# Optimization experiments

Hardware: AMD Instinct MI355X
Metric: run time of the kernel (lower is better)

The kernel has to match this reference:

```python
import jax, jax.numpy as jnp
import numpy as np

H = 16
D_MODEL = 1024
D_K = D_MODEL // H
NEG = -1e9


def setup_inputs() -> dict:
    key = jax.random.key(0)
    ks = jax.random.split(key, 12)
    B, S, D = 2, 2048, D_MODEL
    scale = 1.0 / np.sqrt(D)
    inp = {
        "query": jax.random.normal(ks[0], (B, S, D), jnp.float32),
        "key": jax.random.normal(ks[1], (B, S, D), jnp.float32),
        "value": jax.random.normal(ks[2], (B, S, D), jnp.float32),
        "mask": jax.random.randint(ks[3], (B, S, S), 0, 2, jnp.int32),
        # four Linear(d_model, d_model) layers: q, k, v, out projections
        "Wq": jax.random.normal(ks[4], (D, D), jnp.float32) * scale,
        "bq": jnp.zeros((D,), jnp.float32),
        "Wk": jax.random.normal(ks[5], (D, D), jnp.float32) * scale,
        "bk": jnp.zeros((D,), jnp.float32),
        "Wv": jax.random.normal(ks[6], (D, D), jnp.float32) * scale,
        "bv": jnp.zeros((D,), jnp.float32),
        "Wo": jax.random.normal(ks[7], (D, D), jnp.float32) * scale,
        "bo": jnp.zeros((D,), jnp.float32),
    }
    return inp


def reference(query, key, value, mask, Wq, bq, Wk, bk, Wv, bv, Wo, bo):
    B, S, D = query.shape
    # QKV projections, then split into heads: [B, H, S, D_K]
    def proj(x, W, b):
        return (x @ W + b).reshape(B, S, H, D_K).transpose(0, 2, 1, 3)

    q = proj(query, Wq, bq)
    k = proj(key, Wk, bk)
    v = proj(value, Wv, bv)

    # scaled dot-product attention; scale by sqrt(d_k) (query.size(-1) after split)
    scores = jnp.einsum("bhqd,bhkd->bhqk", q, k) / np.sqrt(D_K)
    scores = jnp.where(mask[:, None, :, :] == 0, NEG, scores)
    p = jax.nn.softmax(scores, axis=-1)  # dropout is identity in eval mode
    x = jnp.einsum("bhqk,bhkd->bhqd", p, v)

    # merge heads and apply output projection
    x = x.transpose(0, 2, 1, 3).reshape(B, S, H * D_K)
    return x @ Wo + bo
```

## Files before the change

### kernel.cpp

```cpp
#include <hip/hip_runtime.h>

typedef _Float16 f16;
typedef __attribute__((ext_vector_type(2))) _Float16 f16x2;
typedef __attribute__((ext_vector_type(4))) _Float16 f16x4;
typedef __attribute__((ext_vector_type(8))) _Float16 f16x8;
typedef __attribute__((ext_vector_type(4))) float f32x4;

#define MFMA16(A_, B_, C_) __builtin_amdgcn_mfma_f32_16x16x32_f16(A_, B_, C_, 0, 0, 0)
#define EXP2(x) __builtin_amdgcn_exp2f(x)

#define NHEAD 16
#define SEQ 2048
#define DM 1024
#define DK 64
#define NBATCH 2
#define M_TOT (NBATCH * SEQ)
#define CSC 0.18033688011112042f

#define GLDS(gp, lp)                                                                     \
    __builtin_amdgcn_global_load_lds((const __attribute__((address_space(1))) void*)(gp), \
                                     (__attribute__((address_space(3))) void*)(lp), 16, 0, 0)

__global__ __launch_bounds__(256) void prep_k(
    const int* __restrict__ mask, unsigned long long* __restrict__ mp,
    const float* __restrict__ xq, const float* __restrict__ xk, const float* __restrict__ xv,
    f16* __restrict__ oq, f16* __restrict__ ok, f16* __restrict__ ov,
    const float* __restrict__ Wq, const float* __restrict__ Wk,
    const float* __restrict__ Wv, const float* __restrict__ Wo, f16* __restrict__ Wt) {
    __shared__ float T[64][65];
    const int z = blockIdx.z, bx = blockIdx.x, tid = threadIdx.x;
    if (z < 3) {
        const float* src = z == 0 ? xq : (z == 1 ? xk : xv);
        f16* dst = z == 0 ? oq : (z == 1 ? ok : ov);
        size_t i = ((size_t)bx * 256 + tid) * 8;
        float4 a = *(const float4*)&src[i];
        float4 b = *(const float4*)&src[i + 4];
        f16x8 h;
        h[0] = (f16)a.x; h[1] = (f16)a.y; h[2] = (f16)a.z; h[3] = (f16)a.w;
        h[4] = (f16)b.x; h[5] = (f16)b.y; h[6] = (f16)b.z; h[7] = (f16)b.w;
        *(f16x8*)&dst[i] = h;
    } else if (z == 3) {
        if (bx >= 1024) return;
        const int zz = bx >> 8, t = bx & 255;
        const float* W = zz == 0 ? Wq : (zz == 1 ? Wk : (zz == 2 ? Wv : Wo));
        const float wsc = zz == 0 ? CSC : 1.0f;
        f16* out = Wt + (size_t)zz * DM * DM;
        const int k0 = (t >> 4) * 64, n0 = (t & 15) * 64;
        const int r = tid >> 2, q = tid & 3;
        const float4* s = (const float4*)&W[(size_t)(k0 + r) * DM + n0 + q * 16];
        float4 v0 = s[0], v1 = s[1], v2 = s[2], v3 = s[3];
        T[r][q * 16 + 0] = v0.x; T[r][q * 16 + 1] = v0.y; T[r][q * 16 + 2] = v0.z; T[r][q * 16 + 3] = v0.w;
        T[r][q * 16 + 4] = v1.x; T[r][q * 16 + 5] = v1.y; T[r][q * 16 + 6] = v1.z; T[r][q * 16 + 7] = v1.w;
        T[r][q * 16 + 8] = v2.x; T[r][q * 16 + 9] = v2.y; T[r][q * 16 + 10] = v2.z; T[r][q * 16 + 11] = v2.w;
        T[r][q * 16 + 12] = v3.x; T[r][q * 16 + 13] = v3.y; T[r][q * 16 + 14] = v3.z; T[r][q * 16 + 15] = v3.w;
        __syncthreads();
        f16x8 h0, h1;
#pragma unroll
        for (int j = 0; j < 8; ++j) {
            h0[j] = (f16)(T[q * 16 + j][r] * wsc);
            h1[j] = (f16)(T[q * 16 + 8 + j][r] * wsc);
        }
        *(f16x8*)&out[(size_t)(n0 + r) * DM + k0 + q * 16] = h0;
        *(f16x8*)&out[(size_t)(n0 + r) * DM + k0 + q * 16 + 8] = h1;
    } else {
        if (bx >= 512) return;
        int lane = tid & 63;
        int gw = (bx * 256 + tid) >> 6;
        const int nw = (512 * 256) >> 6;
        const int nwords = NBATCH * SEQ * (SEQ / 64);
        for (int w = gw; w < nwords; w += nw) {
            int v = mask[(size_t)w * 64 + lane];
            unsigned long long bits = __ballot(v != 0);
            if (lane == 0) mp[w] = bits;
        }
    }
}

__device__ __forceinline__ void gemm_core(const f16* __restrict__ A, const f16* __restrict__ Bt,
                                          int m0, int n0, f16* Al, f16* Bl, f32x4 acc[4][4], int tid) {
    const int lane = tid & 63;
    const int wv = tid >> 6;
    const int wr = wv >> 1, wc = wv & 1;
    const int g = lane >> 4, c = lane & 15;

    for (int k0 = 0; k0 < DM; k0 += 64) {
#pragma unroll
        for (int j = 0; j < 4; ++j) {
            int chunk = j * 256 + tid;
            int row = chunk >> 3, cc = chunk & 7;
            int ccs = cc ^ (row & 7);
            GLDS(&A[(size_t)(m0 + row) * DM + k0 + ccs * 8], &Al[chunk * 8]);
        }
#pragma unroll
        for (int j = 0; j < 4; ++j) {
            int chunk = j * 256 + tid;
            int row = chunk >> 3, cc = chunk & 7;
            int ccs = cc ^ (row & 7);
            GLDS(&Bt[(size_t)(n0 + row) * DM + k0 + ccs * 8], &Bl[chunk * 8]);
        }
        __syncthreads();
#pragma unroll
        for (int ks = 0; ks < 2; ++ks) {
            f16x8 af[4], bf[4];
#pragma unroll
            for (int mi = 0; mi < 4; ++mi) {
                int row = wr * 64 + mi * 16 + c;
                af[mi] = *(const f16x8*)&Al[row * 64 + ((ks * 4 + g) ^ (row & 7)) * 8];
            }
#pragma unroll
            for (int ni = 0; ni < 4; ++ni) {
                int row = wc * 64 + ni * 16 + c;
                bf[ni] = *(const f16x8*)&Bl[row * 64 + ((ks * 4 + g) ^ (row & 7)) * 8];
            }
#pragma unroll
            for (int mi = 0; mi < 4; ++mi)
#pragma unroll
                for (int ni = 0; ni < 4; ++ni)
                    acc[mi][ni] = MFMA16(af[mi], bf[ni], acc[mi][ni]);
        }
        __syncthreads();
    }
}

__device__ __forceinline__ void xcd_swizzle(int& bx, int& by, int gdx) {
    int lin = by * gdx + bx;
    int nl = (lin & 7) * 32 + (lin >> 3);
    bx = nl % gdx;
    by = nl / gdx;
}

__global__ __launch_bounds__(256) void gemm_qkv2_k(
    const f16* __restrict__ Xq, const f16* __restrict__ Xk, const f16* __restrict__ Xv,
    const f16* __restrict__ Wt, const float* __restrict__ bq, const float* __restrict__ bk,
    const float* __restrict__ bv, f16* __restrict__ Qh, f16* __restrict__ Kh, f16* __restrict__ VhT) {
    __shared__ f16 Al[128 * 64];
    __shared__ f16 Bl[128 * 64];
    const int which = blockIdx.z;
    const f16* A = which == 0 ? Xq : (which == 1 ? Xk : Xv);
    const f16* Bt = Wt + (size_t)which * DM * DM;
    const float* bias = which == 0 ? bq : (which == 1 ? bk : bv);

    const int tid = threadIdx.x, lane = tid & 63, wv = tid >> 6;
    const int wr = wv >> 1, wc = wv & 1, g = lane >> 4, c = lane & 15;
    int bx = blockIdx.x, by = blockIdx.y;
    xcd_swizzle(bx, by, gridDim.x);
    const int m0 = by * 128, n0 = bx * 128;

    f32x4 acc[4][4] = {};
    gemm_core(A, Bt, m0, n0, Al, Bl, acc, tid);

    const float bsc = which == 0 ? CSC : 1.0f;
    if (which == 2) {
#pragma unroll
        for (int ni = 0; ni < 4; ++ni) {
            int n = n0 + wc * 64 + ni * 16 + c;
            float bias_n = bias[n];
            int hh = n >> 6, d = n & 63;
#pragma unroll
            for (int mi = 0; mi < 4; ++mi) {
                int mbase = m0 + wr * 64 + mi * 16 + g * 4;
                int bb = mbase >> 11, s = mbase & (SEQ - 1);
                f16x4 o;
#pragma unroll
                for (int r = 0; r < 4; ++r) o[r] = (f16)(acc[mi][ni][r] + bias_n);
                *(f16x4*)&VhT[(((size_t)(bb * NHEAD + hh)) * DK + d) * SEQ + s] = o;
            }
        }
    } else {
        f16* OUT = which == 0 ? Qh : Kh;
#pragma unroll
        for (int ni = 0; ni < 4; ++ni) {
            int n = n0 + wc * 64 + ni * 16 + c;
            float bias_n = bias[n] * bsc;
            int hh = n >> 6, d = n & 63;
#pragma unroll
            for (int mi = 0; mi < 4; ++mi) {
                int mbase = m0 + wr * 64 + mi * 16 + g * 4;
#pragma unroll
                for (int r = 0; r < 4; ++r) {
                    int m = mbase + r;
                    int bb = m >> 11, s = m & (SEQ - 1);
                    OUT[(((size_t)(bb * NHEAD + hh)) * SEQ + s) * DK + d] = (f16)(acc[mi][ni][r] + bias_n);
                }
            }
        }
    }
}

__global__ __launch_bounds__(256) void gemm_out2_k(
    const f16* __restrict__ Xo, const f16* __restrict__ Wto, const float* __restrict__ bo,
    float* __restrict__ OUT) {
    __shared__ f16 Al[128 * 64];
    __shared__ f16 Bl[128 * 64];
    const int tid = threadIdx.x, lane = tid & 63, wv = tid >> 6;
    const int wr = wv >> 1, wc = wv & 1, g = lane >> 4, c = lane & 15;
    int bx = blockIdx.x, by = blockIdx.y;
    xcd_swizzle(bx, by, gridDim.x);
    const int m0 = by * 128, n0 = bx * 128;

    f32x4 acc[4][4] = {};
    gemm_core(Xo, Wto, m0, n0, Al, Bl, acc, tid);

#pragma unroll
    for (int ni = 0; ni < 4; ++ni) {
        int n = n0 + wc * 64 + ni * 16 + c;
        float bias_n = bo[n];
#pragma unroll
        for (int mi = 0; mi < 4; ++mi) {
            int mbase = m0 + wr * 64 + mi * 16 + g * 4;
#pragma unroll
            for (int r = 0; r < 4; ++r) {
                int m = mbase + r;
                OUT[(size_t)m * DM + n] = acc[mi][ni][r] + bias_n;
            }
        }
    }
}

#define QBLK 128
#define NHALF 2
#define KTH (SEQ / 64 / NHALF)

__global__ __launch_bounds__(512) void attn_k(
    const f16* __restrict__ Qh, const f16* __restrict__ Kh, const f16* __restrict__ VhT,
    const unsigned long long* __restrict__ mp, f16* __restrict__ O0, f16* __restrict__ O1,
    float2* __restrict__ ml) {
    __shared__ f16 Kl[2][4096];
    __shared__ f16 Vl[2][4096];

    const int tid = threadIdx.x, lane = tid & 63, wv = tid >> 6;
    const int g = lane >> 4, c = lane & 15;
    const int lin = blockIdx.x;
    const int key = lin & 31;
    const int half = (lin >> 5) & 1;
    const int qt = lin >> 6;
    const int hh = key & (NHEAD - 1), b = key >> 4;
    const size_t headoff = ((size_t)(b * NHEAD + hh)) * SEQ * DK;
    const f16* Qb = Qh + headoff;
    const f16* Kb = Kh + headoff + (size_t)half * (SEQ / NHALF) * DK;
    const f16* VbT = VhT + headoff + (size_t)half * (SEQ / NHALF);

    const int srow = tid >> 3, scc = (tid & 7) ^ (srow & 7);
    const int kap = ((srow >> 4) & 1) * 32 + ((srow >> 2) & 3) * 8 + ((srow >> 5) & 1) * 4 + (srow & 3);

#define STAGE_ATTN(jj, pp)                                                      \
    do {                                                                        \
        GLDS(&Kb[(size_t)((jj)*64 + kap) * DK + scc * 8], &Kl[pp][tid * 8]);    \
        GLDS(&VbT[(size_t)srow * SEQ + (jj)*64 + scc * 8], &Vl[pp][tid * 8]);   \
    } while (0)

    const int qrow = qt * QBLK + wv * 16 + c;
    f16x8 bq0 = *(const f16x8*)&Qb[(size_t)qrow * DK + g * 8];
    f16x8 bq1 = *(const f16x8*)&Qb[(size_t)qrow * DK + 32 + g * 8];

    f32x4 acc[4] = {};
    float l_run = 0.f;

    const unsigned long long* mrow = mp + ((size_t)b * SEQ + qrow) * (SEQ / 64) + half * KTH;
    unsigned long long wq_cur = mrow[0];

    STAGE_ATTN(0, 0);
    int p = 0;
    for (int j = 0; j < KTH; ++j) {
        __syncthreads();
        if (j + 1 < KTH) STAGE_ATTN(j + 1, p ^ 1);
        unsigned long long wq_nxt = (j + 1 < KTH) ? mrow[j + 1] : 0ull;

        f32x4 sc[4];
        __builtin_amdgcn_s_setprio(1);
#pragma unroll
        for (int nk = 0; nk < 4; ++nk) {
            int row = nk * 16 + c;
            f16x8 k0 = *(const f16x8*)&Kl[p][row * 64 + ((g ^ (row & 7)) * 8)];
            f16x8 k1 = *(const f16x8*)&Kl[p][row * 64 + (((4 + g) ^ (row & 7)) * 8)];
            f32x4 z = {};
            z = MFMA16(k0, bq0, z);
            z = MFMA16(k1, bq1, z);
            sc[nk] = z;
        }
        __builtin_amdgcn_s_setprio(0);

        unsigned long long wq_g = wq_cur >> (g * 8);
        float ps = 0.f;
#pragma unroll
        for (int nk = 0; nk < 4; ++nk) {
            unsigned int nib = (unsigned int)(wq_g >> ((nk & 1) * 32 + (nk >> 1) * 4)) & 0xFu;
#pragma unroll
            for (int r = 0; r < 4; ++r) {
                float pp = EXP2(sc[nk][r]);
                pp = (nib & (1u << r)) ? pp : 0.f;
                sc[nk][r] = pp;
                ps += pp;
            }
        }
        l_run += ps;

        f16x8 pb0, pb1;
#pragma unroll
        for (int j2 = 0; j2 < 2; ++j2)
#pragma unroll
            for (int r = 0; r < 4; ++r) {
                pb0[j2 * 4 + r] = (f16)sc[j2 * 2][r];
                pb1[j2 * 4 + r] = (f16)sc[j2 * 2 + 1][r];
            }

        __builtin_amdgcn_s_setprio(1);
#pragma unroll
        for (int nd = 0; nd < 4; ++nd) {
            int row = nd * 16 + c;
            f16x8 v0 = *(const f16x8*)&Vl[p][row * 64 + ((g ^ (row & 7)) * 8)];
            f16x8 v1 = *(const f16x8*)&Vl[p][row * 64 + (((4 + g) ^ (row & 7)) * 8)];
            acc[nd] = MFMA16(v0, pb0, acc[nd]);
            acc[nd] = MFMA16(v1, pb1, acc[nd]);
        }
        __builtin_amdgcn_s_setprio(0);

        wq_cur = wq_nxt;
        p ^= 1;
    }

    l_run += __shfl_xor(l_run, 16);
    l_run += __shfl_xor(l_run, 32);

    f16* Opart = half ? O1 : O0;
    {
        float inv = l_run > 0.f ? 1.0f / l_run : 0.f;
        size_t hrow = headoff / DK + qrow;
#pragma unroll
        for (int nd = 0; nd < 4; ++nd) {
            f16x4 o;
#pragma unroll
            for (int r = 0; r < 4; ++r) o[r] = (f16)(acc[nd][r] * inv);
            *(f16x4*)&Opart[hrow * DK + nd * 16 + g * 4] = o;
        }
        if (g == 0) ml[(size_t)half * (M_TOT * NHEAD) + hrow] = make_float2(0.f, l_run);
    }
#undef STAGE_ATTN
}

__global__ __launch_bounds__(256) void combine_k(const f16* __restrict__ O0, const f16* __restrict__ O1,
                                                 const float2* __restrict__ ml, f16* __restrict__ Xo) {
    const int row = blockIdx.x * 32 + (threadIdx.x >> 3);
    const int d0 = (threadIdx.x & 7) * 8;
    const int b = row >> 15, hh = (row >> 11) & 15, q = row & (SEQ - 1);
    float2 a = ml[row];
    float2 bb = ml[(M_TOT * NHEAD) + row];
    float m = fmaxf(a.x, bb.x);
    float w0 = a.y * EXP2(a.x - m);
    float w1 = bb.y * EXP2(bb.x - m);
    float inv = 1.0f / (w0 + w1);
    float a0 = w0 * inv, a1 = w1 * inv;
    f16x8 o0 = *(const f16x8*)&O0[(size_t)row * DK + d0];
    f16x8 o1 = *(const f16x8*)&O1[(size_t)row * DK + d0];
    f16x8 o;
#pragma unroll
    for (int i = 0; i < 8; ++i) o[i] = (f16)(a0 * (float)o0[i] + a1 * (float)o1[i]);
    *(f16x8*)&Xo[((size_t)(b * SEQ + q)) * DM + hh * DK + d0] = o;
}

extern "C" void kernel_launch(void* const* d_in, const int* in_sizes, int n_in,
                              void* d_out, int out_size, void* d_ws, size_t ws_size,
                              hipStream_t stream) {
    const float* query = (const float*)d_in[0];
    const float* key_ = (const float*)d_in[1];
    const float* value = (const float*)d_in[2];
    const int* mask = (const int*)d_in[3];
    const float* Wq = (const float*)d_in[4];
    const float* bq = (const float*)d_in[5];
    const float* Wk = (const float*)d_in[6];
    const float* bk = (const float*)d_in[7];
    const float* Wv = (const float*)d_in[8];
    const float* bv = (const float*)d_in[9];
    const float* Wo = (const float*)d_in[10];
    const float* bo = (const float*)d_in[11];
    float* out = (float*)d_out;

    char* ws = (char*)d_ws;
    const size_t headsz = (size_t)NBATCH * NHEAD * SEQ * DK * sizeof(f16);
    unsigned long long* mp = (unsigned long long*)(ws);
    f16* Qh = (f16*)(ws + (1 << 20));
    f16* Kh = (f16*)(ws + (1 << 20) + headsz);
    f16* VhT = (f16*)(ws + (1 << 20) + 2 * headsz);
    f16* Xhq = (f16*)(ws + (1 << 20) + 3 * headsz);
    f16* Xhk = (f16*)(ws + (1 << 20) + 4 * headsz);
    f16* Xhv = (f16*)(ws + (1 << 20) + 5 * headsz);
    f16* Wt = (f16*)(ws + (1 << 20) + 6 * headsz);
    float2* ml = (float2*)(ws + (1 << 20) + 7 * headsz);
    f16* Xo = Xhq;

    hipLaunchKernelGGL(prep_k, dim3(M_TOT * DM / (8 * 256), 1, 5), dim3(256), 0, stream,
                       mask, mp, query, key_, value, Xhq, Xhk, Xhv, Wq, Wk, Wv, Wo, Wt);
    hipLaunchKernelGGL(gemm_qkv2_k, dim3(DM / 128, M_TOT / 128, 3), dim3(256), 0, stream,
                       Xhq, Xhk, Xhv, Wt, bq, bk, bv, Qh, Kh, VhT);
    hipLaunchKernelGGL(attn_k, dim3(SEQ / QBLK * NHEAD * NBATCH * NHALF), dim3(512), 0, stream,
                       Qh, Kh, VhT, mp, Xhk, Xhv, ml);
    hipLaunchKernelGGL(combine_k, dim3(M_TOT * NHEAD / 32), dim3(256), 0, stream, Xhk, Xhv, ml, Xo);
    hipLaunchKernelGGL(gemm_out2_k, dim3(DM / 128, M_TOT / 128), dim3(256), 0, stream,
                       Xo, Wt + (size_t)3 * DM * DM, bo, out);
}
```

Baseline: 159.1 us.

## Process two 16-row query tiles per wave to reuse K/V LDS tiles

Each wave now computes attention for 32 query rows (two interleaved 16-row tiles) instead of 16, doubling the query block per workgroup to 256. Each K and V fragment read from LDS feeds twice as many MFMAs, which cuts LDS reads and staging per unit of work and raises instruction-level parallelism. In exchange, register use roughly doubles for accumulators and scores, and the grid has half as many blocks, which may reduce occupancy and load balance across CUs.

```diff
diff --git a/kernel.cpp b/kernel.cpp
--- a/kernel.cpp
+++ b/kernel.cpp
@@ -217,11 +217,11 @@
     }
 }
 
-#define QBLK 128
+#define QBLK 256
 #define NHALF 2
 #define KTH (SEQ / 64 / NHALF)
 
-__global__ __launch_bounds__(512) void attn_k(
+__global__ __launch_bounds__(512, 4) void attn_k(
     const f16* __restrict__ Qh, const f16* __restrict__ Kh, const f16* __restrict__ VhT,
     const unsigned long long* __restrict__ mp, f16* __restrict__ O0, f16* __restrict__ O1,
     float2* __restrict__ ml) {
@@ -249,24 +249,29 @@
         GLDS(&VbT[(size_t)srow * SEQ + (jj)*64 + scc * 8], &Vl[pp][tid * 8]);   \
     } while (0)
 
-    const int qrow = qt * QBLK + wv * 16 + c;
-    f16x8 bq0 = *(const f16x8*)&Qb[(size_t)qrow * DK + g * 8];
-    f16x8 bq1 = *(const f16x8*)&Qb[(size_t)qrow * DK + 32 + g * 8];
-
-    f32x4 acc[4] = {};
-    float l_run = 0.f;
-
-    const unsigned long long* mrow = mp + ((size_t)b * SEQ + qrow) * (SEQ / 64) + half * KTH;
-    unsigned long long wq_cur = mrow[0];
+    const int qrowA = qt * QBLK + wv * 32 + c;
+    const int qrowB = qrowA + 16;
+    f16x8 bqA0 = *(const f16x8*)&Qb[(size_t)qrowA * DK + g * 8];
+    f16x8 bqA1 = *(const f16x8*)&Qb[(size_t)qrowA * DK + 32 + g * 8];
+    f16x8 bqB0 = *(const f16x8*)&Qb[(size_t)qrowB * DK + g * 8];
+    f16x8 bqB1 = *(const f16x8*)&Qb[(size_t)qrowB * DK + 32 + g * 8];
+
+    f32x4 accA[4] = {}, accB[4] = {};
+    float lA = 0.f, lB = 0.f;
+
+    const unsigned long long* mrowA = mp + ((size_t)b * SEQ + qrowA) * (SEQ / 64) + half * KTH;
+    const unsigned long long* mrowB = mp + ((size_t)b * SEQ + qrowB) * (SEQ / 64) + half * KTH;
+    unsigned long long wqA = mrowA[0], wqB = mrowB[0];
 
     STAGE_ATTN(0, 0);
     int p = 0;
     for (int j = 0; j < KTH; ++j) {
         __syncthreads();
         if (j + 1 < KTH) STAGE_ATTN(j + 1, p ^ 1);
-        unsigned long long wq_nxt = (j + 1 < KTH) ? mrow[j + 1] : 0ull;
-
-        f32x4 sc[4];
+        unsigned long long wqA_n = (j + 1 < KTH) ? mrowA[j + 1] : 0ull;
+        unsigned long long wqB_n = (j + 1 < KTH) ? mrowB[j + 1] : 0ull;
+
+        f32x4 sA[4], sB[4];
         __builtin_amdgcn_s_setprio(1);
 #pragma unroll
         for (int nk = 0; nk < 4; ++nk) {
@@ -274,34 +279,46 @@
             f16x8 k0 = *(const f16x8*)&Kl[p][row * 64 + ((g ^ (row & 7)) * 8)];
             f16x8 k1 = *(const f16x8*)&Kl[p][row * 64 + (((4 + g) ^ (row & 7)) * 8)];
             f32x4 z = {};
-            z = MFMA16(k0, bq0, z);
-            z = MFMA16(k1, bq1, z);
-            sc[nk] = z;
+            z = MFMA16(k0, bqA0, z);
+            z = MFMA16(k1, bqA1, z);
+            sA[nk] = z;
+            f32x4 y = {};
+            y = MFMA16(k0, bqB0, y);
+            y = MFMA16(k1, bqB1, y);
+            sB[nk] = y;
         }
         __builtin_amdgcn_s_setprio(0);
 
-        unsigned long long wq_g = wq_cur >> (g * 8);
-        float ps = 0.f;
+        unsigned long long wgA = wqA >> (g * 8), wgB = wqB >> (g * 8);
+        float psA = 0.f, psB = 0.f;
 #pragma unroll
         for (int nk = 0; nk < 4; ++nk) {
-            unsigned int nib = (unsigned int)(wq_g >> ((nk & 1) * 32 + (nk >> 1) * 4)) & 0xFu;
+            unsigned int nibA = (unsigned int)(wgA >> ((nk & 1) * 32 + (nk >> 1) * 4)) & 0xFu;
+            unsigned int nibB = (unsigned int)(wgB >> ((nk & 1) * 32 + (nk >> 1) * 4)) & 0xFu;
 #pragma unroll
             for (int r = 0; r < 4; ++r) {
-                float pp = EXP2(sc[nk][r]);
-                pp = (nib & (1u << r)) ? pp : 0.f;
-                sc[nk][r] = pp;
-                ps += pp;
-            }
-        }
-        l_run += ps;
-
-        f16x8 pb0, pb1;
+                float pa = EXP2(sA[nk][r]);
+                pa = (nibA & (1u << r)) ? pa : 0.f;
+                sA[nk][r] = pa;
+                psA += pa;
+                float pb = EXP2(sB[nk][r]);
+                pb = (nibB & (1u << r)) ? pb : 0.f;
+                sB[nk][r] = pb;
+                psB += pb;
+            }
+        }
+        lA += psA;
+        lB += psB;
+
+        f16x8 pA0, pA1, pB0, pB1;
 #pragma unroll
         for (int j2 = 0; j2 < 2; ++j2)
 #pragma unroll
             for (int r = 0; r < 4; ++r) {
-                pb0[j2 * 4 + r] = (f16)sc[j2 * 2][r];
-                pb1[j2 * 4 + r] = (f16)sc[j2 * 2 + 1][r];
+                pA0[j2 * 4 + r] = (f16)sA[j2 * 2][r];
+                pA1[j2 * 4 + r] = (f16)sA[j2 * 2 + 1][r];
+                pB0[j2 * 4 + r] = (f16)sB[j2 * 2][r];
+                pB1[j2 * 4 + r] = (f16)sB[j2 * 2 + 1][r];
             }
 
         __builtin_amdgcn_s_setprio(1);
@@ -310,30 +327,44 @@
             int row = nd * 16 + c;
             f16x8 v0 = *(const f16x8*)&Vl[p][row * 64 + ((g ^ (row & 7)) * 8)];
             f16x8 v1 = *(const f16x8*)&Vl[p][row * 64 + (((4 + g) ^ (row & 7)) * 8)];
-            acc[nd] = MFMA16(v0, pb0, acc[nd]);
-            acc[nd] = MFMA16(v1, pb1, acc[nd]);
+            accA[nd] = MFMA16(v0, pA0, accA[nd]);
+            accA[nd] = MFMA16(v1, pA1, accA[nd]);
+            accB[nd] = MFMA16(v0, pB0, accB[nd]);
+            accB[nd] = MFMA16(v1, pB1, accB[nd]);
         }
         __builtin_amdgcn_s_setprio(0);
 
-        wq_cur = wq_nxt;
+        wqA = wqA_n;
+        wqB = wqB_n;
         p ^= 1;
     }
 
-    l_run += __shfl_xor(l_run, 16);
-    l_run += __shfl_xor(l_run, 32);
+    lA += __shfl_xor(lA, 16);
+    lA += __shfl_xor(lA, 32);
+    lB += __shfl_xor(lB, 16);
+    lB += __shfl_xor(lB, 32);
 
     f16* Opart = half ? O1 : O0;
     {
-        float inv = l_run > 0.f ? 1.0f / l_run : 0.f;
-        size_t hrow = headoff / DK + qrow;
+        float invA = lA > 0.f ? 1.0f / lA : 0.f;
+        float invB = lB > 0.f ? 1.0f / lB : 0.f;
+        size_t hrowA = headoff / DK + qrowA;
+        size_t hrowB = headoff / DK + qrowB;
 #pragma unroll
         for (int nd = 0; nd < 4; ++nd) {
-            f16x4 o;
-#pragma unroll
-            for (int r = 0; r < 4; ++r) o[r] = (f16)(acc[nd][r] * inv);
-            *(f16x4*)&Opart[hrow * DK + nd * 16 + g * 4] = o;
-        }
-        if (g == 0) ml[(size_t)half * (M_TOT * NHEAD) + hrow] = make_float2(0.f, l_run);
+            f16x4 oA, oB;
+#pragma unroll
+            for (int r = 0; r < 4; ++r) {
+                oA[r] = (f16)(accA[nd][r] * invA);
+                oB[r] = (f16)(accB[nd][r] * invB);
+            }
+            *(f16x4*)&Opart[hrowA * DK + nd * 16 + g * 4] = oA;
+            *(f16x4*)&Opart[hrowB * DK + nd * 16 + g * 4] = oB;
+        }
+        if (g == 0) {
+            ml[(size_t)half * (M_TOT * NHEAD) + hrowA] = make_float2(0.f, lA);
+            ml[(size_t)half * (M_TOT * NHEAD) + hrowB] = make_float2(0.f, lB);
+        }
     }
 #undef STAGE_ATTN
 }
```

Measured after the change: 159.5 us. No clear change (+0.2%).
